# Optimization experiments

Measured on AMD Instinct MI355X. Metric: run time of the kernel, lower is better.

The kernel has to match this reference:

```python
import jax, jax.numpy as jnp
import numpy as np

L, N, E, D = 4, 50000, 250000, 128
EPS = 1e-5

def _ln(h, g, b):
    mu = jnp.mean(h, axis=-1, keepdims=True)
    var = jnp.mean(jnp.square(h - mu), axis=-1, keepdims=True)
    return (h - mu) * jax.lax.rsqrt(var + EPS) * g + b

def setup_inputs() -> dict:
    key = jax.random.key(0)
    ks = jax.random.split(key, 8)
    s1 = 1.0 / np.sqrt(3 * D)
    s2 = 1.0 / np.sqrt(D)
    s3 = 1.0 / np.sqrt(2 * D)
    return {
        "x": jax.random.normal(ks[0], (N, D), jnp.float32),
        "edge_index": jax.random.randint(ks[1], (2, E), 0, N, jnp.int32),
        "edge_attr": jax.random.normal(ks[2], (E, D), jnp.float32),
        "eW1": jax.random.normal(ks[3], (L, 3 * D, D), jnp.float32) * s1,
        "eb1": jnp.zeros((L, D), jnp.float32),
        "eW2": jax.random.normal(ks[4], (L, D, D), jnp.float32) * s2,
        "eb2": jnp.zeros((L, D), jnp.float32),
        "eG": jnp.ones((L, D), jnp.float32),
        "eB": jnp.zeros((L, D), jnp.float32),
        "nW1": jax.random.normal(ks[5], (L, 2 * D, D), jnp.float32) * s3,
        "nb1": jnp.zeros((L, D), jnp.float32),
        "nW2": jax.random.normal(ks[6], (L, D, D), jnp.float32) * s2,
        "nb2": jnp.zeros((L, D), jnp.float32),
        "nG": jnp.ones((L, D), jnp.float32),
        "nB": jnp.zeros((L, D), jnp.float32),
    }

def reference(x, edge_index, edge_attr, eW1, eb1, eW2, eb2, eG, eB,
              nW1, nb1, nW2, nb2, nG, nB):
    src = edge_index[0]  # scatter target (custom aggregate uses edge_index[0])
    dst = edge_index[1]  # x_i under PyG source_to_target flow
    n_nodes = x.shape[0]

    def step(carry, p):
        xc, ea = carry
        ew1, eb1_, ew2, eb2_, eg, ebt, nw1, nb1_, nw2, nb2_, ng, nbt = p
        # message: cat(x_i, x_j, edge_attr) -> MLP -> residual
        m = jnp.concatenate([xc[dst], xc[src], ea], axis=1)  # [E, 3D]
        h = jax.nn.relu(m @ ew1 + eb1_) @ ew2 + eb2_
        ea_new = ea + _ln(h, eg, ebt)
        # aggregate: scatter-sum edges into nodes by edge_index[0]
        agg = jax.ops.segment_sum(ea_new, src, num_segments=n_nodes)  # [N, D]
        # update: cat(x, agg) -> MLP -> residual
        u = jnp.concatenate([xc, agg], axis=1)  # [N, 2D]
        h2 = jax.nn.relu(u @ nw1 + nb1_) @ nw2 + nb2_
        x_new = xc + _ln(h2, ng, nbt)
        return (x_new, ea_new), None

    (x_out, ea_out), _ = jax.lax.scan(
        step, (x, edge_attr),
        (eW1, eb1, eW2, eb2, eG, eB, nW1, nb1, nW2, nb2, nG, nB))
    return x_out, ea_out
```

## Files before the change

kernel.cpp:

```cpp
#include <hip/hip_runtime.h>
#include <hip/hip_bf16.h>

#define N_NODES 50000
#define N_EDGES 250000
#define DIM 128
#define LAYERS 4
#define LN_EPS 1e-5f

typedef __hip_bfloat16 bf16;
typedef float f32x4 __attribute__((ext_vector_type(4)));
typedef __bf16 bfx8 __attribute__((ext_vector_type(8)));
typedef unsigned short u16x8 __attribute__((ext_vector_type(8)));
typedef unsigned short u16x4 __attribute__((ext_vector_type(4)));
typedef unsigned int   u32x4 __attribute__((ext_vector_type(4)));

#define F_X   0
#define F_EA  1
#define F_EW1 2
#define F_EW2 3
#define F_EG  4
#define F_NW1 5
#define F_NW2 6
#define F_NG  7

__device__ __forceinline__ float b2f(bf16 v) { return __bfloat162float(v); }
__device__ __forceinline__ bf16  f2b(float v) { return __float2bfloat16(v); }
__device__ __forceinline__ unsigned short f2us(float v) {
    return __builtin_bit_cast(unsigned short, __float2bfloat16(v));
}
__device__ __forceinline__ float us2f(unsigned short u) {
    return __builtin_bit_cast(float, (unsigned)u << 16);
}

__device__ __forceinline__ float ldv(const void* p, size_t i, int f) {
    if (f) return ((const float*)p)[i];
    else   return b2f(((const bf16*)p)[i]);
}
__device__ __forceinline__ void stv(void* p, size_t i, float v, int f) {
    if (f) ((float*)p)[i] = v;
    else   ((bf16*)p)[i] = f2b(v);
}

__device__ __forceinline__ bfx8 cvt8(f32x4 lo, f32x4 hi) {
    u16x8 u;
    #pragma unroll
    for (int i = 0; i < 4; i++) { u[i] = f2us(lo[i]); u[i + 4] = f2us(hi[i]); }
    return __builtin_bit_cast(bfx8, u);
}

__device__ __forceinline__ void mfma8(const bf16* pBk, bfx8 a, f32x4* acc) {
    #pragma unroll
    for (int f = 0; f < 8; f++) {
        bfx8 b = *reinterpret_cast<const bfx8*>(pBk + f * 128);
        acc[f] = __builtin_amdgcn_mfma_f32_16x16x32_bf16(a, b, acc[f], 0, 0, 0);
    }
}

__global__ void k_detect(const void* x, const void* ea,
                         const void* eW1, const void* eW2,
                         const void* nW1, const void* nW2,
                         const void* eG, const void* nG,
                         int* flags)
{
    __shared__ int bad[6];
    const void* ptrs[6] = { x, ea, eW1, eW2, nW1, nW2 };
    const int t = threadIdx.x;
    if (t < 6) bad[t] = 0;
    __syncthreads();
    for (int b = 0; b < 6; b++) {
        const bf16* p = (const bf16*)ptrs[b];
        int isbad = 0;
        for (int i = t; i < 4096; i += 256) {
            float v = b2f(p[i]);
            if (!(fabsf(v) < 1e4f)) isbad = 1;
        }
        if (isbad) atomicOr(&bad[b], 1);
    }
    __syncthreads();
    if (t == 0) {
        flags[F_X]   = bad[0];
        flags[F_EA]  = bad[1];
        flags[F_EW1] = bad[2];
        flags[F_EW2] = bad[3];
        flags[F_NW1] = bad[4];
        flags[F_NW2] = bad[5];
        const bf16* g1 = (const bf16*)eG;
        const bf16* g2 = (const bf16*)nG;
        flags[F_EG] = (b2f(g1[0]) == 1.0f && b2f(g1[1]) == 1.0f) ? 0 : 1;
        flags[F_NG] = (b2f(g2[0]) == 1.0f && b2f(g2[1]) == 1.0f) ? 0 : 1;
    }
}

__global__ void k_init_x(const void* __restrict__ x_in, float* __restrict__ xf,
                         bf16* __restrict__ xb, const int* __restrict__ flags) {
    const int f = flags[F_X];
    size_t i = ((size_t)blockIdx.x * 256 + threadIdx.x) * 4;
    if (i >= (size_t)N_NODES * DIM) return;
    f32x4 v;
    if (f) {
        v = *(const f32x4*)((const float*)x_in + i);
    } else {
        u16x4 u = *(const u16x4*)((const unsigned short*)x_in + i);
        #pragma unroll
        for (int q = 0; q < 4; q++) v[q] = us2f(u[q]);
    }
    *(f32x4*)(xf + i) = v;
    u16x4 ub;
    #pragma unroll
    for (int q = 0; q < 4; q++) ub[q] = f2us(v[q]);
    *(u16x4*)((unsigned short*)xb + i) = ub;
}

__global__ void k_init_ea(const void* __restrict__ ea_in, void* __restrict__ d_out,
                          const int* __restrict__ flags) {
    const int fe = flags[F_EA];
    const int fo = flags[F_X];
    size_t i = ((size_t)blockIdx.x * 256 + threadIdx.x) * 4;
    if (i >= (size_t)N_EDGES * DIM) return;
    if (fe == fo) {
        if (fo) {
            float* d = (float*)d_out + (size_t)N_NODES * DIM;
            *(u32x4*)(d + i) = *(const u32x4*)((const float*)ea_in + i);
        } else {
            bf16* d = (bf16*)d_out + (size_t)N_NODES * DIM;
            *(u16x4*)((unsigned short*)d + i) =
                *(const u16x4*)((const unsigned short*)ea_in + i);
        }
    } else {
        f32x4 v;
        if (fe) v = *(const f32x4*)((const float*)ea_in + i);
        else {
            u16x4 u = *(const u16x4*)((const unsigned short*)ea_in + i);
            #pragma unroll
            for (int q = 0; q < 4; q++) v[q] = us2f(u[q]);
        }
        if (fo) {
            float* d = (float*)d_out + (size_t)N_NODES * DIM;
            *(f32x4*)(d + i) = v;
        } else {
            bf16* d = (bf16*)d_out + (size_t)N_NODES * DIM;
            u16x4 ub;
            #pragma unroll
            for (int q = 0; q < 4; q++) ub[q] = f2us(v[q]);
            *(u16x4*)((unsigned short*)d + i) = ub;
        }
    }
}

__global__ void k_wprep(const void* __restrict__ W, bf16* __restrict__ Wb,
                        int K, const int* __restrict__ flags, int fidx)
{
    const int f = flags[fidx];
    size_t i = (size_t)blockIdx.x * 256 + threadIdx.x;
    const int per = K * DIM;
    if (i >= (size_t)LAYERS * per) return;
    int l   = (int)(i / per);
    int rem = (int)(i % per);
    int j   = rem & 7;
    int c   = (rem >> 3) & 127;
    int kq  = rem >> 10;
    int k   = kq * 8 + j;
    Wb[i] = f2b(ldv(W, (size_t)l * per + (size_t)k * DIM + c, f));
}

__global__ void k_deg(const int* __restrict__ srcI, int* __restrict__ deg) {
    int e = blockIdx.x * 256 + threadIdx.x;
    if (e < N_EDGES) atomicAdd(&deg[srcI[e]], 1);
}

#define SCH ((N_NODES + 255) / 256)
__global__ void k_scan(const int* __restrict__ deg, int* __restrict__ off,
                       int* __restrict__ cur) {
    __shared__ int part[256];
    const int t = threadIdx.x;
    const int lo = t * SCH;
    const int hi = (lo + SCH < N_NODES) ? (lo + SCH) : N_NODES;
    int s = 0;
    for (int i = lo; i < hi; i++) s += deg[i];
    part[t] = s;
    __syncthreads();
    if (t == 0) {
        int run = 0;
        for (int i = 0; i < 256; i++) { int v = part[i]; part[i] = run; run += v; }
    }
    __syncthreads();
    int run = part[t];
    for (int i = lo; i < hi; i++) { off[i] = run; cur[i] = run; run += deg[i]; }
    if (hi == N_NODES) off[N_NODES] = run;
}

__global__ void k_fill(const int* __restrict__ srcI, int* __restrict__ cur,
                       int* __restrict__ lst) {
    int e = blockIdx.x * 256 + threadIdx.x;
    if (e < N_EDGES) {
        int p = atomicAdd(&cur[srcI[e]], 1);
        lst[p] = e;
    }
}

__global__ __launch_bounds__(256)
void k_edge(const bf16* __restrict__ xb,
            void* __restrict__ d_out,
            const int* __restrict__ srcI, const int* __restrict__ dstI,
            const bf16* __restrict__ W1b, const bf16* __restrict__ W2b,
            const void* __restrict__ b1, const void* __restrict__ b2,
            const void* __restrict__ G,  const void* __restrict__ B,
            const int* __restrict__ flags, int layer)
{
    __shared__ alignas(16) float smem[4][16 * 132];

    const int fo = flags[F_X];
    const int fg = flags[F_EG];

    void* ea = fo ? (void*)((float*)d_out + (size_t)N_NODES * DIM)
                  : (void*)((bf16*)d_out + (size_t)N_NODES * DIM);

    const bf16* W1l = W1b + (size_t)layer * 3 * DIM * DIM;
    const bf16* W2l = W2b + (size_t)layer * DIM * DIM;
    const bf16* b1l = (const bf16*)b1 + (size_t)layer * DIM;
    const bf16* b2l = (const bf16*)b2 + (size_t)layer * DIM;
    const bf16* Bl  = (const bf16*)B  + (size_t)layer * DIM;
    const void* Gl  = fg ? (const void*)((const float*)G + (size_t)layer * DIM)
                         : (const void*)((const bf16*)G  + (size_t)layer * DIM);

    const int tid  = threadIdx.x;
    const int wv   = tid >> 6;
    const int lane = tid & 63;
    const int cl   = lane & 15;
    const int kp   = lane >> 4;

    const int e0w = blockIdx.x * 64 + wv * 16;
    const int eA  = (e0w + cl < N_EDGES) ? (e0w + cl) : (N_EDGES - 1);
    const bf16* pAd = xb + (size_t)dstI[eA] * DIM + kp * 8;
    const bf16* pAs = xb + (size_t)srcI[eA] * DIM + kp * 8;
    const bf16* pB  = W1l + kp * 1024 + cl * 8;

    f32x4 acc[8];
    #pragma unroll
    for (int f = 0; f < 8; f++) acc[f] = (f32x4){0.f, 0.f, 0.f, 0.f};

    #pragma unroll
    for (int kk = 0; kk < 4; kk++)
        mfma8(pB + (size_t)kk * 4096,
              *reinterpret_cast<const bfx8*>(pAd + kk * 32), acc);
    #pragma unroll
    for (int kk = 0; kk < 4; kk++)
        mfma8(pB + (size_t)(kk + 4) * 4096,
              *reinterpret_cast<const bfx8*>(pAs + kk * 32), acc);
    if (fo) {
        const float* pAe = (const float*)ea + (size_t)eA * DIM + kp * 8;
        #pragma unroll
        for (int kk = 0; kk < 4; kk++) {
            f32x4 lo = *reinterpret_cast<const f32x4*>(pAe + kk * 32);
            f32x4 hi = *reinterpret_cast<const f32x4*>(pAe + kk * 32 + 4);
            mfma8(pB + (size_t)(kk + 8) * 4096, cvt8(lo, hi), acc);
        }
    } else {
        const bf16* pAe = (const bf16*)ea + (size_t)eA * DIM + kp * 8;
        #pragma unroll
        for (int kk = 0; kk < 4; kk++)
            mfma8(pB + (size_t)(kk + 8) * 4096,
                  *reinterpret_cast<const bfx8*>(pAe + kk * 32), acc);
    }

    char* hb = (char*)&smem[wv][0];
    #pragma unroll
    for (int f = 0; f < 8; f++) {
        const int col = f * 16 + cl;
        const float bias1 = b2f(b1l[col]);
        #pragma unroll
        for (int j = 0; j < 4; j++) {
            const int r = kp * 4 + j;
            float hv = fmaxf(acc[f][j] + bias1, 0.f);
            *(bf16*)(hb + r * 256 + ((col * 2) ^ ((r & 7) << 4))) = f2b(hv);
        }
    }

    const bf16* pB2 = W2l + kp * 1024 + cl * 8;
    f32x4 acc2[8];
    #pragma unroll
    for (int f = 0; f < 8; f++) acc2[f] = (f32x4){0.f, 0.f, 0.f, 0.f};
    #pragma unroll
    for (int kk = 0; kk < 4; kk++) {
        bfx8 a = *reinterpret_cast<const bfx8*>(
            hb + cl * 256 + ((kk * 64 + kp * 16) ^ ((cl & 7) << 4)));
        mfma8(pB2 + (size_t)kk * 4096, a, acc2);
    }

    float g_[8], be_[8];
    #pragma unroll
    for (int f = 0; f < 8; f++) {
        const int col = f * 16 + cl;
        const float bias2 = b2f(b2l[col]);
        #pragma unroll
        for (int j = 0; j < 4; j++) acc2[f][j] += bias2;
        g_[f]  = ldv(Gl, col, fg);
        be_[f] = b2f(Bl[col]);
    }
    float mu[4], rs[4];
    #pragma unroll
    for (int j = 0; j < 4; j++) {
        float s = 0.f, q = 0.f;
        #pragma unroll
        for (int f = 0; f < 8; f++) { float v = acc2[f][j]; s += v; q += v * v; }
        #pragma unroll
        for (int m = 1; m <= 8; m <<= 1) { s += __shfl_xor(s, m); q += __shfl_xor(q, m); }
        mu[j] = s * (1.f / DIM);
        float var = q * (1.f / DIM) - mu[j] * mu[j];
        rs[j] = rsqrtf(var + LN_EPS);
    }

    float* vs = &smem[wv][0];
    #pragma unroll
    for (int f = 0; f < 8; f++) {
        #pragma unroll
        for (int j = 0; j < 4; j++) {
            const float val = (acc2[f][j] - mu[j]) * rs[j] * g_[f] + be_[f];
            vs[(kp * 4 + j) * 132 + f * 16 + cl] = val;
        }
    }
    const int lr = lane >> 5;
    const int lc = (lane & 31) * 4;
    #pragma unroll
    for (int i = 0; i < 8; i++) {
        const int r2 = 2 * i + lr;
        const int e  = e0w + r2;
        if (e >= N_EDGES) continue;
        f32x4 v = *(const f32x4*)&vs[r2 * 132 + lc];
        const size_t off = (size_t)e * DIM + lc;
        if (fo) {
            float* pe = (float*)ea + off;
            f32x4 o = *(const f32x4*)pe;
            *(f32x4*)pe = o + v;
        } else {
            bf16* pe = (bf16*)ea + off;
            u16x4 uo = *(const u16x4*)(unsigned short*)pe;
            u16x4 un;
            #pragma unroll
            for (int q = 0; q < 4; q++) un[q] = f2us(us2f(uo[q]) + v[q]);
            *(u16x4*)(unsigned short*)pe = un;
        }
    }
}

__global__ __launch_bounds__(256)
void k_node(float* __restrict__ xf, bf16* __restrict__ xb,
            void* __restrict__ d_out,
            const int* __restrict__ off_, const int* __restrict__ lst,
            const bf16* __restrict__ W1b, const bf16* __restrict__ W2b,
            const void* __restrict__ b1, const void* __restrict__ b2,
            const void* __restrict__ G,  const void* __restrict__ B,
            const int* __restrict__ flags, int layer)
{
    __shared__ alignas(16) float smem[4][16 * 132];

    const int fo = flags[F_X];
    const int fg = flags[F_NG];

    const bf16* W1l = W1b + (size_t)layer * 2 * DIM * DIM;
    const bf16* W2l = W2b + (size_t)layer * DIM * DIM;
    const bf16* b1l = (const bf16*)b1 + (size_t)layer * DIM;
    const bf16* b2l = (const bf16*)b2 + (size_t)layer * DIM;
    const bf16* Bl  = (const bf16*)B  + (size_t)layer * DIM;
    const void* Gl  = fg ? (const void*)((const float*)G + (size_t)layer * DIM)
                         : (const void*)((const bf16*)G  + (size_t)layer * DIM);

    const int tid  = threadIdx.x;
    const int wv   = tid >> 6;
    const int lane = tid & 63;
    const int cl   = lane & 15;
    const int kp   = lane >> 4;

    const int n0w = blockIdx.x * 64 + wv * 16;
    const int nA  = (n0w + cl < N_NODES) ? (n0w + cl) : (N_NODES - 1);

    f32x4 agl[4], agh[4];
    #pragma unroll
    for (int kk = 0; kk < 4; kk++) {
        agl[kk] = (f32x4){0.f, 0.f, 0.f, 0.f};
        agh[kk] = (f32x4){0.f, 0.f, 0.f, 0.f};
    }
    {
        const int beg = off_[nA], end = off_[nA + 1];
        if (fo) {
            const float* base = (const float*)d_out + (size_t)N_NODES * DIM;
            for (int idx = beg; idx < end; ++idx) {
                const int e = lst[idx];
                const float* p = base + (size_t)e * DIM + kp * 8;
                #pragma unroll
                for (int kk = 0; kk < 4; kk++) {
                    agl[kk] += *(const f32x4*)(p + kk * 32);
                    agh[kk] += *(const f32x4*)(p + kk * 32 + 4);
                }
            }
        } else {
            const bf16* base = (const bf16*)d_out + (size_t)N_NODES * DIM;
            for (int idx = beg; idx < end; ++idx) {
                const int e = lst[idx];
                const bf16* p = base + (size_t)e * DIM + kp * 8;
                #pragma unroll
                for (int kk = 0; kk < 4; kk++) {
                    u16x8 u = *(const u16x8*)(const unsigned short*)(p + kk * 32);
                    #pragma unroll
                    for (int q = 0; q < 4; q++) {
                        agl[kk][q] += us2f(u[q]);
                        agh[kk][q] += us2f(u[q + 4]);
                    }
                }
            }
        }
    }

    const bf16* pAx = xb + (size_t)nA * DIM + kp * 8;
    const bf16* pB  = W1l + kp * 1024 + cl * 8;

    f32x4 acc[8];
    #pragma unroll
    for (int f = 0; f < 8; f++) acc[f] = (f32x4){0.f, 0.f, 0.f, 0.f};

    #pragma unroll
    for (int kk = 0; kk < 4; kk++)
        mfma8(pB + (size_t)kk * 4096,
              *reinterpret_cast<const bfx8*>(pAx + kk * 32), acc);
    #pragma unroll
    for (int kk = 0; kk < 4; kk++)
        mfma8(pB + (size_t)(kk + 4) * 4096, cvt8(agl[kk], agh[kk]), acc);

    char* hb = (char*)&smem[wv][0];
    #pragma unroll
    for (int f = 0; f < 8; f++) {
        const int col = f * 16 + cl;
        const float bias1 = b2f(b1l[col]);
        #pragma unroll
        for (int j = 0; j < 4; j++) {
            const int r = kp * 4 + j;
            float hv = fmaxf(acc[f][j] + bias1, 0.f);
            *(bf16*)(hb + r * 256 + ((col * 2) ^ ((r & 7) << 4))) = f2b(hv);
        }
    }

    const bf16* pB2 = W2l + kp * 1024 + cl * 8;
    f32x4 acc2[8];
    #pragma unroll
    for (int f = 0; f < 8; f++) acc2[f] = (f32x4){0.f, 0.f, 0.f, 0.f};
    #pragma unroll
    for (int kk = 0; kk < 4; kk++) {
        bfx8 a = *reinterpret_cast<const bfx8*>(
            hb + cl * 256 + ((kk * 64 + kp * 16) ^ ((cl & 7) << 4)));
        mfma8(pB2 + (size_t)kk * 4096, a, acc2);
    }

    float g_[8], be_[8];
    #pragma unroll
    for (int f = 0; f < 8; f++) {
        const int col = f * 16 + cl;
        const float bias2 = b2f(b2l[col]);
        #pragma unroll
        for (int j = 0; j < 4; j++) acc2[f][j] += bias2;
        g_[f]  = ldv(Gl, col, fg);
        be_[f] = b2f(Bl[col]);
    }
    float mu[4], rs[4];
    #pragma unroll
    for (int j = 0; j < 4; j++) {
        float s = 0.f, q = 0.f;
        #pragma unroll
        for (int f = 0; f < 8; f++) { float v = acc2[f][j]; s += v; q += v * v; }
        #pragma unroll
        for (int m = 1; m <= 8; m <<= 1) { s += __shfl_xor(s, m); q += __shfl_xor(q, m); }
        mu[j] = s * (1.f / DIM);
        float var = q * (1.f / DIM) - mu[j] * mu[j];
        rs[j] = rsqrtf(var + LN_EPS);
    }

    float* vs = &smem[wv][0];
    #pragma unroll
    for (int f = 0; f < 8; f++) {
        #pragma unroll
        for (int j = 0; j < 4; j++) {
            const float val = (acc2[f][j] - mu[j]) * rs[j] * g_[f] + be_[f];
            vs[(kp * 4 + j) * 132 + f * 16 + cl] = val;
        }
    }
    const bool wout = (layer == LAYERS - 1);
    const int lr = lane >> 5;
    const int lc = (lane & 31) * 4;
    #pragma unroll
    for (int i = 0; i < 8; i++) {
        const int r2 = 2 * i + lr;
        const int n2 = n0w + r2;
        if (n2 >= N_NODES) continue;
        f32x4 v = *(const f32x4*)&vs[r2 * 132 + lc];
        const size_t off = (size_t)n2 * DIM + lc;
        f32x4 xo = *(const f32x4*)&xf[off];
        f32x4 xn = xo + v;
        *(f32x4*)&xf[off] = xn;
        u16x4 ub;
        #pragma unroll
        for (int q = 0; q < 4; q++) ub[q] = f2us(xn[q]);
        *(u16x4*)((unsigned short*)xb + off) = ub;
        if (wout) {
            if (fo) *(f32x4*)((float*)d_out + off) = xn;
            else    *(u16x4*)((unsigned short*)(bf16*)d_out + off) = ub;
        }
    }
}

extern "C" void kernel_launch(void* const* d_in, const int* in_sizes, int n_in,
                              void* d_out, int out_size, void* d_ws, size_t ws_size,
                              hipStream_t stream)
{
    (void)in_sizes; (void)n_in; (void)out_size; (void)ws_size;
    const void* x_in  = d_in[0];
    const int*  ei    = (const int*)d_in[1];
    const void* ea_in = d_in[2];
    const void* eW1 = d_in[3];  const void* eb1 = d_in[4];
    const void* eW2 = d_in[5];  const void* eb2 = d_in[6];
    const void* eG  = d_in[7];  const void* eB  = d_in[8];
    const void* nW1 = d_in[9];  const void* nb1 = d_in[10];
    const void* nW2 = d_in[11]; const void* nb2 = d_in[12];
    const void* nG  = d_in[13]; const void* nB  = d_in[14];

    char* ws = (char*)d_ws;
    int* flags = (int*)ws;
    char* p = ws + 256;
    float* xf  = (float*)p;  p += (size_t)N_NODES * DIM * 4;
    bf16*  xb  = (bf16*)p;   p += (size_t)N_NODES * DIM * 2;
    bf16*  eW1b = (bf16*)p;  p += (size_t)LAYERS * 3 * DIM * DIM * 2;
    bf16*  eW2b = (bf16*)p;  p += (size_t)LAYERS * DIM * DIM * 2;
    bf16*  nW1b = (bf16*)p;  p += (size_t)LAYERS * 2 * DIM * DIM * 2;
    bf16*  nW2b = (bf16*)p;  p += (size_t)LAYERS * DIM * DIM * 2;
    int* deg     = (int*)p;  p += 200000;
    int* csr_off = (int*)p;  p += 200016;
    int* cur     = (int*)p;  p += 200000;
    int* lst     = (int*)p;  p += 1000000;

    const int* srcI = ei;
    const int* dstI = ei + N_EDGES;

    k_detect<<<1, 256, 0, stream>>>(x_in, ea_in, eW1, eW2, nW1, nW2, eG, nG, flags);
    k_init_x<<<(N_NODES * DIM / 4 + 255) / 256, 256, 0, stream>>>(x_in, xf, xb, flags);
    k_init_ea<<<(int)(((size_t)N_EDGES * DIM / 4 + 255) / 256), 256, 0, stream>>>(ea_in, d_out, flags);
    k_wprep<<<(LAYERS * 3 * DIM * DIM + 255) / 256, 256, 0, stream>>>(eW1, eW1b, 3 * DIM, flags, F_EW1);
    k_wprep<<<(LAYERS * DIM * DIM + 255) / 256, 256, 0, stream>>>(eW2, eW2b, DIM, flags, F_EW2);
    k_wprep<<<(LAYERS * 2 * DIM * DIM + 255) / 256, 256, 0, stream>>>(nW1, nW1b, 2 * DIM, flags, F_NW1);
    k_wprep<<<(LAYERS * DIM * DIM + 255) / 256, 256, 0, stream>>>(nW2, nW2b, DIM, flags, F_NW2);

    hipMemsetAsync(deg, 0, N_NODES * sizeof(int), stream);
    k_deg<<<(N_EDGES + 255) / 256, 256, 0, stream>>>(srcI, deg);
    k_scan<<<1, 256, 0, stream>>>(deg, csr_off, cur);
    k_fill<<<(N_EDGES + 255) / 256, 256, 0, stream>>>(srcI, cur, lst);

    for (int l = 0; l < LAYERS; l++) {
        k_edge<<<(N_EDGES + 63) / 64, 256, 0, stream>>>(
            xb, d_out, srcI, dstI, eW1b, eW2b, eb1, eb2, eG, eB, flags, l);
        k_node<<<(N_NODES + 63) / 64, 256, 0, stream>>>(
            xf, xb, d_out, csr_off, lst, nW1b, nW2b, nb1, nb2, nG, nB, flags, l);
    }
}
```

Before: 1.392 ms.

## Write edge outputs in CSR-sorted bf16 copy for contiguous node aggregation

The edge kernel now also writes each updated edge feature, rounded to bf16, into an extra buffer at its CSR position. The node kernel can then stream each node's incoming edges contiguously instead of gathering through an index list. The old edge-attribute values are also prefetched at the start of the edge kernel so their latency overlaps the matmuls. In exchange the edge kernel does an extra scattered bf16 write, uses more workspace, and in fp32 mode the node aggregation now sums bf16-rounded values, which costs precision.

After: 2.069 ms. +48.6%, slower.

```diff
diff --git a/kernel.cpp b/kernel.cpp
--- a/kernel.cpp
+++ b/kernel.cpp
@@ -190,11 +190,11 @@
 }
 
 __global__ void k_fill(const int* __restrict__ srcI, int* __restrict__ cur,
-                       int* __restrict__ lst) {
+                       int* __restrict__ pos) {
     int e = blockIdx.x * 256 + threadIdx.x;
     if (e < N_EDGES) {
         int p = atomicAdd(&cur[srcI[e]], 1);
-        lst[p] = e;
+        pos[e] = p;
     }
 }
 
@@ -202,6 +202,7 @@
 void k_edge(const bf16* __restrict__ xb,
             void* __restrict__ d_out,
             const int* __restrict__ srcI, const int* __restrict__ dstI,
+            const int* __restrict__ pos,  bf16* __restrict__ eac,
             const bf16* __restrict__ W1b, const bf16* __restrict__ W2b,
             const void* __restrict__ b1, const void* __restrict__ b2,
             const void* __restrict__ G,  const void* __restrict__ B,
@@ -214,6 +215,28 @@
 
     void* ea = fo ? (void*)((float*)d_out + (size_t)N_NODES * DIM)
                   : (void*)((bf16*)d_out + (size_t)N_NODES * DIM);
+
+    const int tid  = threadIdx.x;
+    const int wv   = tid >> 6;
+    const int lane = tid & 63;
+    const int cl   = lane & 15;
+    const int kp   = lane >> 4;
+
+    const int e0w = blockIdx.x * 64 + wv * 16;
+
+    const int lr = lane >> 5;
+    const int lc = (lane & 31) * 4;
+    f32x4 eaof[8];
+    u16x4 eaob[8];
+    int   posR[8];
+    #pragma unroll
+    for (int i = 0; i < 8; i++) {
+        const int e = e0w + 2 * i + lr;
+        const int ec = (e < N_EDGES) ? e : (N_EDGES - 1);
+        posR[i] = pos[ec];
+        if (fo) eaof[i] = *(const f32x4*)((const float*)ea + (size_t)ec * DIM + lc);
+        else    eaob[i] = *(const u16x4*)((const unsigned short*)ea + (size_t)ec * DIM + lc);
+    }
 
     const bf16* W1l = W1b + (size_t)layer * 3 * DIM * DIM;
     const bf16* W2l = W2b + (size_t)layer * DIM * DIM;
@@ -223,13 +246,6 @@
     const void* Gl  = fg ? (const void*)((const float*)G + (size_t)layer * DIM)
                          : (const void*)((const bf16*)G  + (size_t)layer * DIM);
 
-    const int tid  = threadIdx.x;
-    const int wv   = tid >> 6;
-    const int lane = tid & 63;
-    const int cl   = lane & 15;
-    const int kp   = lane >> 4;
-
-    const int e0w = blockIdx.x * 64 + wv * 16;
     const int eA  = (e0w + cl < N_EDGES) ? (e0w + cl) : (N_EDGES - 1);
     const bf16* pAd = xb + (size_t)dstI[eA] * DIM + kp * 8;
     const bf16* pAs = xb + (size_t)srcI[eA] * DIM + kp * 8;
@@ -319,8 +335,6 @@
             vs[(kp * 4 + j) * 132 + f * 16 + cl] = val;
         }
     }
-    const int lr = lane >> 5;
-    const int lc = (lane & 31) * 4;
     #pragma unroll
     for (int i = 0; i < 8; i++) {
         const int r2 = 2 * i + lr;
@@ -328,25 +342,26 @@
         if (e >= N_EDGES) continue;
         f32x4 v = *(const f32x4*)&vs[r2 * 132 + lc];
         const size_t off = (size_t)e * DIM + lc;
+        f32x4 nw;
         if (fo) {
-            float* pe = (float*)ea + off;
-            f32x4 o = *(const f32x4*)pe;
-            *(f32x4*)pe = o + v;
+            nw = eaof[i] + v;
+            *(f32x4*)((float*)ea + off) = nw;
         } else {
-            bf16* pe = (bf16*)ea + off;
-            u16x4 uo = *(const u16x4*)(unsigned short*)pe;
-            u16x4 un;
             #pragma unroll
-            for (int q = 0; q < 4; q++) un[q] = f2us(us2f(uo[q]) + v[q]);
-            *(u16x4*)(unsigned short*)pe = un;
-        }
+            for (int q = 0; q < 4; q++) nw[q] = us2f(eaob[i][q]) + v[q];
+        }
+        u16x4 ub;
+        #pragma unroll
+        for (int q = 0; q < 4; q++) ub[q] = f2us(nw[q]);
+        if (!fo) *(u16x4*)((unsigned short*)ea + off) = ub;
+        *(u16x4*)((unsigned short*)eac + (size_t)posR[i] * DIM + lc) = ub;
     }
 }
 
 __global__ __launch_bounds__(256)
 void k_node(float* __restrict__ xf, bf16* __restrict__ xb,
             void* __restrict__ d_out,
-            const int* __restrict__ off_, const int* __restrict__ lst,
+            const int* __restrict__ off_, const bf16* __restrict__ eac,
             const bf16* __restrict__ W1b, const bf16* __restrict__ W2b,
             const void* __restrict__ b1, const void* __restrict__ b2,
             const void* __restrict__ G,  const void* __restrict__ B,
@@ -382,30 +397,16 @@
     }
     {
         const int beg = off_[nA], end = off_[nA + 1];
-        if (fo) {
-            const float* base = (const float*)d_out + (size_t)N_NODES * DIM;
-            for (int idx = beg; idx < end; ++idx) {
-                const int e = lst[idx];
-                const float* p = base + (size_t)e * DIM + kp * 8;
+        const unsigned short* pr =
+            (const unsigned short*)eac + (size_t)beg * DIM + kp * 8;
+        for (int idx = beg; idx < end; ++idx, pr += DIM) {
+            #pragma unroll
+            for (int kk = 0; kk < 4; kk++) {
+                u16x8 u = *(const u16x8*)(pr + kk * 32);
                 #pragma unroll
-                for (int kk = 0; kk < 4; kk++) {
-                    agl[kk] += *(const f32x4*)(p + kk * 32);
-                    agh[kk] += *(const f32x4*)(p + kk * 32 + 4);
-                }
-            }
-        } else {
-            const bf16* base = (const bf16*)d_out + (size_t)N_NODES * DIM;
-            for (int idx = beg; idx < end; ++idx) {
-                const int e = lst[idx];
-                const bf16* p = base + (size_t)e * DIM + kp * 8;
-                #pragma unroll
-                for (int kk = 0; kk < 4; kk++) {
-                    u16x8 u = *(const u16x8*)(const unsigned short*)(p + kk * 32);
-                    #pragma unroll
-                    for (int q = 0; q < 4; q++) {
-                        agl[kk][q] += us2f(u[q]);
-                        agh[kk][q] += us2f(u[q + 4]);
-                    }
+                for (int q = 0; q < 4; q++) {
+                    agl[kk][q] += us2f(u[q]);
+                    agh[kk][q] += us2f(u[q + 4]);
                 }
             }
         }
@@ -533,7 +534,8 @@
     int* deg     = (int*)p;  p += 200000;
     int* csr_off = (int*)p;  p += 200016;
     int* cur     = (int*)p;  p += 200000;
-    int* lst     = (int*)p;  p += 1000000;
+    int* pos     = (int*)p;  p += 1000000;
+    bf16* eac    = (bf16*)p; p += (size_t)N_EDGES * DIM * 2;
 
     const int* srcI = ei;
     const int* dstI = ei + N_EDGES;
@@ -549,12 +551,12 @@
     hipMemsetAsync(deg, 0, N_NODES * sizeof(int), stream);
     k_deg<<<(N_EDGES + 255) / 256, 256, 0, stream>>>(srcI, deg);
     k_scan<<<1, 256, 0, stream>>>(deg, csr_off, cur);
-    k_fill<<<(N_EDGES + 255) / 256, 256, 0, stream>>>(srcI, cur, lst);
+    k_fill<<<(N_EDGES + 255) / 256, 256, 0, stream>>>(srcI, cur, pos);
 
     for (int l = 0; l < LAYERS; l++) {
         k_edge<<<(N_EDGES + 63) / 64, 256, 0, stream>>>(
-            xb, d_out, srcI, dstI, eW1b, eW2b, eb1, eb2, eG, eB, flags, l);
+            xb, d_out, srcI, dstI, pos, eac, eW1b, eW2b, eb1, eb2, eG, eB, flags, l);
         k_node<<<(N_NODES + 63) / 64, 256, 0, stream>>>(
-            xf, xb, d_out, csr_off, lst, nW1b, nW2b, nb1, nb2, nG, nB, flags, l);
-    }
-}
+            xf, xb, d_out, csr_off, eac, nW1b, nW2b, nb1, nb2, nG, nB, flags, l);
+    }
+}
```

## Store edge features in CSR-sorted order so node aggregation reads contiguously

Applied to the files above, without the earlier changes.

Edge attributes are permuted into a float32 workspace sorted by scatter target (CSR order), with src/dst indices permuted to match. The node kernel now sums a contiguous run of rows instead of gathering rows through the edge list, and the edge kernel writes results back in sorted order. The final layer scatters results back to the original edge order in the output. This adds a permutation pass, extra workspace, and a scattered write on the last layer, and it keeps edge state in fp32 even when the output is bf16.

Result: slower. 1.972 ms (+41.6%).

```diff
diff --git a/kernel.cpp b/kernel.cpp
--- a/kernel.cpp
+++ b/kernel.cpp
@@ -35,10 +35,6 @@
 __device__ __forceinline__ float ldv(const void* p, size_t i, int f) {
     if (f) return ((const float*)p)[i];
     else   return b2f(((const bf16*)p)[i]);
-}
-__device__ __forceinline__ void stv(void* p, size_t i, float v, int f) {
-    if (f) ((float*)p)[i] = v;
-    else   ((bf16*)p)[i] = f2b(v);
 }
 
 __device__ __forceinline__ bfx8 cvt8(f32x4 lo, f32x4 hi) {
@@ -111,40 +107,24 @@
     *(u16x4*)((unsigned short*)xb + i) = ub;
 }
 
-__global__ void k_init_ea(const void* __restrict__ ea_in, void* __restrict__ d_out,
+__global__ void k_init_ea(const void* __restrict__ ea_in, float* __restrict__ eaw,
+                          const int* __restrict__ lst,
                           const int* __restrict__ flags) {
     const int fe = flags[F_EA];
-    const int fo = flags[F_X];
     size_t i = ((size_t)blockIdx.x * 256 + threadIdx.x) * 4;
     if (i >= (size_t)N_EDGES * DIM) return;
-    if (fe == fo) {
-        if (fo) {
-            float* d = (float*)d_out + (size_t)N_NODES * DIM;
-            *(u32x4*)(d + i) = *(const u32x4*)((const float*)ea_in + i);
-        } else {
-            bf16* d = (bf16*)d_out + (size_t)N_NODES * DIM;
-            *(u16x4*)((unsigned short*)d + i) =
-                *(const u16x4*)((const unsigned short*)ea_in + i);
-        }
-    } else {
-        f32x4 v;
-        if (fe) v = *(const f32x4*)((const float*)ea_in + i);
-        else {
-            u16x4 u = *(const u16x4*)((const unsigned short*)ea_in + i);
-            #pragma unroll
-            for (int q = 0; q < 4; q++) v[q] = us2f(u[q]);
-        }
-        if (fo) {
-            float* d = (float*)d_out + (size_t)N_NODES * DIM;
-            *(f32x4*)(d + i) = v;
-        } else {
-            bf16* d = (bf16*)d_out + (size_t)N_NODES * DIM;
-            u16x4 ub;
-            #pragma unroll
-            for (int q = 0; q < 4; q++) ub[q] = f2us(v[q]);
-            *(u16x4*)((unsigned short*)d + i) = ub;
-        }
-    }
+    const int p   = (int)(i >> 7);
+    const int col = (int)(i & 127);
+    const int e   = lst[p];
+    const size_t si = (size_t)e * DIM + col;
+    f32x4 v;
+    if (fe) v = *(const f32x4*)((const float*)ea_in + si);
+    else {
+        u16x4 u = *(const u16x4*)((const unsigned short*)ea_in + si);
+        #pragma unroll
+        for (int q = 0; q < 4; q++) v[q] = us2f(u[q]);
+    }
+    *(f32x4*)(eaw + i) = v;
 }
 
 __global__ void k_wprep(const void* __restrict__ W, bf16* __restrict__ Wb,
@@ -198,10 +178,23 @@
     }
 }
 
+__global__ void k_perm(const int* __restrict__ srcI, const int* __restrict__ dstI,
+                       const int* __restrict__ lst,
+                       int* __restrict__ srcP, int* __restrict__ dstP) {
+    int p = blockIdx.x * 256 + threadIdx.x;
+    if (p < N_EDGES) {
+        const int e = lst[p];
+        srcP[p] = srcI[e];
+        dstP[p] = dstI[e];
+    }
+}
+
 __global__ __launch_bounds__(256)
 void k_edge(const bf16* __restrict__ xb,
+            float* __restrict__ eaw,
             void* __restrict__ d_out,
-            const int* __restrict__ srcI, const int* __restrict__ dstI,
+            const int* __restrict__ srcP, const int* __restrict__ dstP,
+            const int* __restrict__ lst,
             const bf16* __restrict__ W1b, const bf16* __restrict__ W2b,
             const void* __restrict__ b1, const void* __restrict__ b2,
             const void* __restrict__ G,  const void* __restrict__ B,
@@ -211,9 +204,6 @@
 
     const int fo = flags[F_X];
     const int fg = flags[F_EG];
-
-    void* ea = fo ? (void*)((float*)d_out + (size_t)N_NODES * DIM)
-                  : (void*)((bf16*)d_out + (size_t)N_NODES * DIM);
 
     const bf16* W1l = W1b + (size_t)layer * 3 * DIM * DIM;
     const bf16* W2l = W2b + (size_t)layer * DIM * DIM;
@@ -230,9 +220,11 @@
     const int kp   = lane >> 4;
 
     const int e0w = blockIdx.x * 64 + wv * 16;
-    const int eA  = (e0w + cl < N_EDGES) ? (e0w + cl) : (N_EDGES - 1);
-    const bf16* pAd = xb + (size_t)dstI[eA] * DIM + kp * 8;
-    const bf16* pAs = xb + (size_t)srcI[eA] * DIM + kp * 8;
+
+    const int pA  = (e0w + cl < N_EDGES) ? (e0w + cl) : (N_EDGES - 1);
+    const bf16* pAd = xb + (size_t)dstP[pA] * DIM + kp * 8;
+    const bf16* pAs = xb + (size_t)srcP[pA] * DIM + kp * 8;
+    const float* pAe = eaw + (size_t)pA * DIM + kp * 8;
     const bf16* pB  = W1l + kp * 1024 + cl * 8;
 
     f32x4 acc[8];
@@ -247,20 +239,11 @@
     for (int kk = 0; kk < 4; kk++)
         mfma8(pB + (size_t)(kk + 4) * 4096,
               *reinterpret_cast<const bfx8*>(pAs + kk * 32), acc);
-    if (fo) {
-        const float* pAe = (const float*)ea + (size_t)eA * DIM + kp * 8;
-        #pragma unroll
-        for (int kk = 0; kk < 4; kk++) {
-            f32x4 lo = *reinterpret_cast<const f32x4*>(pAe + kk * 32);
-            f32x4 hi = *reinterpret_cast<const f32x4*>(pAe + kk * 32 + 4);
-            mfma8(pB + (size_t)(kk + 8) * 4096, cvt8(lo, hi), acc);
-        }
-    } else {
-        const bf16* pAe = (const bf16*)ea + (size_t)eA * DIM + kp * 8;
-        #pragma unroll
-        for (int kk = 0; kk < 4; kk++)
-            mfma8(pB + (size_t)(kk + 8) * 4096,
-                  *reinterpret_cast<const bfx8*>(pAe + kk * 32), acc);
+    #pragma unroll
+    for (int kk = 0; kk < 4; kk++) {
+        f32x4 lo = *reinterpret_cast<const f32x4*>(pAe + kk * 32);
+        f32x4 hi = *reinterpret_cast<const f32x4*>(pAe + kk * 32 + 4);
+        mfma8(pB + (size_t)(kk + 8) * 4096, cvt8(lo, hi), acc);
     }
 
     char* hb = (char*)&smem[wv][0];
@@ -319,26 +302,31 @@
             vs[(kp * 4 + j) * 132 + f * 16 + cl] = val;
         }
     }
+    const bool last = (layer == LAYERS - 1);
     const int lr = lane >> 5;
     const int lc = (lane & 31) * 4;
     #pragma unroll
     for (int i = 0; i < 8; i++) {
         const int r2 = 2 * i + lr;
-        const int e  = e0w + r2;
-        if (e >= N_EDGES) continue;
+        const int p  = e0w + r2;
+        if (p >= N_EDGES) continue;
         f32x4 v = *(const f32x4*)&vs[r2 * 132 + lc];
-        const size_t off = (size_t)e * DIM + lc;
-        if (fo) {
-            float* pe = (float*)ea + off;
-            f32x4 o = *(const f32x4*)pe;
-            *(f32x4*)pe = o + v;
-        } else {
-            bf16* pe = (bf16*)ea + off;
-            u16x4 uo = *(const u16x4*)(unsigned short*)pe;
-            u16x4 un;
-            #pragma unroll
-            for (int q = 0; q < 4; q++) un[q] = f2us(us2f(uo[q]) + v[q]);
-            *(u16x4*)(unsigned short*)pe = un;
+        float* pe = eaw + (size_t)p * DIM + lc;
+        f32x4 o = *(const f32x4*)pe;
+        f32x4 nw = o + v;
+        *(f32x4*)pe = nw;
+        if (last) {
+            const size_t off = (size_t)lst[p] * DIM + lc;
+            if (fo) {
+                float* d = (float*)d_out + (size_t)N_NODES * DIM;
+                *(f32x4*)(d + off) = nw;
+            } else {
+                bf16* d = (bf16*)d_out + (size_t)N_NODES * DIM;
+                u16x4 ub;
+                #pragma unroll
+                for (int q = 0; q < 4; q++) ub[q] = f2us(nw[q]);
+                *(u16x4*)((unsigned short*)d + off) = ub;
+            }
         }
     }
 }
@@ -346,7 +334,7 @@
 __global__ __launch_bounds__(256)
 void k_node(float* __restrict__ xf, bf16* __restrict__ xb,
             void* __restrict__ d_out,
-            const int* __restrict__ off_, const int* __restrict__ lst,
+            const int* __restrict__ off_, const float* __restrict__ eaw,
             const bf16* __restrict__ W1b, const bf16* __restrict__ W2b,
             const void* __restrict__ b1, const void* __restrict__ b2,
             const void* __restrict__ G,  const void* __restrict__ B,
@@ -382,31 +370,12 @@
     }
     {
         const int beg = off_[nA], end = off_[nA + 1];
-        if (fo) {
-            const float* base = (const float*)d_out + (size_t)N_NODES * DIM;
-            for (int idx = beg; idx < end; ++idx) {
-                const int e = lst[idx];
-                const float* p = base + (size_t)e * DIM + kp * 8;
-                #pragma unroll
-                for (int kk = 0; kk < 4; kk++) {
-                    agl[kk] += *(const f32x4*)(p + kk * 32);
-                    agh[kk] += *(const f32x4*)(p + kk * 32 + 4);
-                }
-            }
-        } else {
-            const bf16* base = (const bf16*)d_out + (size_t)N_NODES * DIM;
-            for (int idx = beg; idx < end; ++idx) {
-                const int e = lst[idx];
-                const bf16* p = base + (size_t)e * DIM + kp * 8;
-                #pragma unroll
-                for (int kk = 0; kk < 4; kk++) {
-                    u16x8 u = *(const u16x8*)(const unsigned short*)(p + kk * 32);
-                    #pragma unroll
-                    for (int q = 0; q < 4; q++) {
-                        agl[kk][q] += us2f(u[q]);
-                        agh[kk][q] += us2f(u[q + 4]);
-                    }
-                }
+        const float* pr = eaw + (size_t)beg * DIM + kp * 8;
+        for (int idx = beg; idx < end; ++idx, pr += DIM) {
+            #pragma unroll
+            for (int kk = 0; kk < 4; kk++) {
+                agl[kk] += *(const f32x4*)(pr + kk * 32);
+                agh[kk] += *(const f32x4*)(pr + kk * 32 + 4);
             }
         }
     }
@@ -534,13 +503,16 @@
     int* csr_off = (int*)p;  p += 200016;
     int* cur     = (int*)p;  p += 200000;
     int* lst     = (int*)p;  p += 1000000;
+    int* srcP    = (int*)p;  p += 1000000;
+    int* dstP    = (int*)p;  p += 1000000;
+    p = (char*)(((size_t)p + 255) & ~(size_t)255);
+    float* eaw   = (float*)p; p += (size_t)N_EDGES * DIM * 4;
 
     const int* srcI = ei;
     const int* dstI = ei + N_EDGES;
 
     k_detect<<<1, 256, 0, stream>>>(x_in, ea_in, eW1, eW2, nW1, nW2, eG, nG, flags);
     k_init_x<<<(N_NODES * DIM / 4 + 255) / 256, 256, 0, stream>>>(x_in, xf, xb, flags);
-    k_init_ea<<<(int)(((size_t)N_EDGES * DIM / 4 + 255) / 256), 256, 0, stream>>>(ea_in, d_out, flags);
     k_wprep<<<(LAYERS * 3 * DIM * DIM + 255) / 256, 256, 0, stream>>>(eW1, eW1b, 3 * DIM, flags, F_EW1);
     k_wprep<<<(LAYERS * DIM * DIM + 255) / 256, 256, 0, stream>>>(eW2, eW2b, DIM, flags, F_EW2);
     k_wprep<<<(LAYERS * 2 * DIM * DIM + 255) / 256, 256, 0, stream>>>(nW1, nW1b, 2 * DIM, flags, F_NW1);
@@ -550,11 +522,13 @@
     k_deg<<<(N_EDGES + 255) / 256, 256, 0, stream>>>(srcI, deg);
     k_scan<<<1, 256, 0, stream>>>(deg, csr_off, cur);
     k_fill<<<(N_EDGES + 255) / 256, 256, 0, stream>>>(srcI, cur, lst);
+    k_perm<<<(N_EDGES + 255) / 256, 256, 0, stream>>>(srcI, dstI, lst, srcP, dstP);
+    k_init_ea<<<(int)(((size_t)N_EDGES * DIM / 4 + 255) / 256), 256, 0, stream>>>(ea_in, eaw, lst, flags);
 
     for (int l = 0; l < LAYERS; l++) {
         k_edge<<<(N_EDGES + 63) / 64, 256, 0, stream>>>(
-            xb, d_out, srcI, dstI, eW1b, eW2b, eb1, eb2, eG, eB, flags, l);
+            xb, eaw, d_out, srcP, dstP, lst, eW1b, eW2b, eb1, eb2, eG, eB, flags, l);
         k_node<<<(N_NODES + 63) / 64, 256, 0, stream>>>(
-            xf, xb, d_out, csr_off, lst, nW1b, nW2b, nb1, nb2, nG, nB, flags, l);
-    }
-}
+            xf, xb, d_out, csr_off, eaw, nW1b, nW2b, nb1, nb2, nG, nB, flags, l);
+    }
+}
```

## Process two edge tiles per wave and stage node aggregation through LDS

Applied to the files above, without the earlier changes.

The edge kernel now handles 32 edges per wave, issuing two MFMA chains for each weight fragment. Each loaded W1/W2 fragment is reused twice, which halves weight traffic per edge at the cost of more accumulator registers and possibly lower occupancy. The node kernel now loads the block's contiguous CSR range of edge rows into shared memory in chunks of 64, with coalesced row loads and block-wide barriers. Each wave then sums its nodes' rows from LDS instead of doing per-lane scattered global gathers. The ea init kernel's same-type copy branch is also folded into the general convert path.

Measured after the change: 1.971 ms. 1.42x slower.

```diff
diff --git a/kernel.cpp b/kernel.cpp
--- a/kernel.cpp
+++ b/kernel.cpp
@@ -53,6 +53,16 @@
     for (int f = 0; f < 8; f++) {
         bfx8 b = *reinterpret_cast<const bfx8*>(pBk + f * 128);
         acc[f] = __builtin_amdgcn_mfma_f32_16x16x32_bf16(a, b, acc[f], 0, 0, 0);
+    }
+}
+
+__device__ __forceinline__ void mfma8d(const bf16* pBk, bfx8 a0, bfx8 a1,
+                                       f32x4* acc0, f32x4* acc1) {
+    #pragma unroll
+    for (int f = 0; f < 8; f++) {
+        bfx8 b = *reinterpret_cast<const bfx8*>(pBk + f * 128);
+        acc0[f] = __builtin_amdgcn_mfma_f32_16x16x32_bf16(a0, b, acc0[f], 0, 0, 0);
+        acc1[f] = __builtin_amdgcn_mfma_f32_16x16x32_bf16(a1, b, acc1[f], 0, 0, 0);
     }
 }
 
@@ -117,33 +127,22 @@
     const int fo = flags[F_X];
     size_t i = ((size_t)blockIdx.x * 256 + threadIdx.x) * 4;
     if (i >= (size_t)N_EDGES * DIM) return;
-    if (fe == fo) {
-        if (fo) {
-            float* d = (float*)d_out + (size_t)N_NODES * DIM;
-            *(u32x4*)(d + i) = *(const u32x4*)((const float*)ea_in + i);
-        } else {
-            bf16* d = (bf16*)d_out + (size_t)N_NODES * DIM;
-            *(u16x4*)((unsigned short*)d + i) =
-                *(const u16x4*)((const unsigned short*)ea_in + i);
-        }
+    f32x4 v;
+    if (fe) v = *(const f32x4*)((const float*)ea_in + i);
+    else {
+        u16x4 u = *(const u16x4*)((const unsigned short*)ea_in + i);
+        #pragma unroll
+        for (int q = 0; q < 4; q++) v[q] = us2f(u[q]);
+    }
+    if (fo) {
+        float* d = (float*)d_out + (size_t)N_NODES * DIM;
+        *(f32x4*)(d + i) = v;
     } else {
-        f32x4 v;
-        if (fe) v = *(const f32x4*)((const float*)ea_in + i);
-        else {
-            u16x4 u = *(const u16x4*)((const unsigned short*)ea_in + i);
-            #pragma unroll
-            for (int q = 0; q < 4; q++) v[q] = us2f(u[q]);
-        }
-        if (fo) {
-            float* d = (float*)d_out + (size_t)N_NODES * DIM;
-            *(f32x4*)(d + i) = v;
-        } else {
-            bf16* d = (bf16*)d_out + (size_t)N_NODES * DIM;
-            u16x4 ub;
-            #pragma unroll
-            for (int q = 0; q < 4; q++) ub[q] = f2us(v[q]);
-            *(u16x4*)((unsigned short*)d + i) = ub;
-        }
+        bf16* d = (bf16*)d_out + (size_t)N_NODES * DIM;
+        u16x4 ub;
+        #pragma unroll
+        for (int q = 0; q < 4; q++) ub[q] = f2us(v[q]);
+        *(u16x4*)((unsigned short*)d + i) = ub;
     }
 }
 
@@ -198,124 +197,28 @@
     }
 }
 
-__global__ __launch_bounds__(256)
-void k_edge(const bf16* __restrict__ xb,
-            void* __restrict__ d_out,
-            const int* __restrict__ srcI, const int* __restrict__ dstI,
-            const bf16* __restrict__ W1b, const bf16* __restrict__ W2b,
-            const void* __restrict__ b1, const void* __restrict__ b2,
-            const void* __restrict__ G,  const void* __restrict__ B,
-            const int* __restrict__ flags, int layer)
+__device__ __forceinline__ void edge_epi(
+    f32x4 (&c2)[8], const float* g_, const float* be_,
+    float* vs, void* ea, int fo, int e_base,
+    int lane, int cl, int kp)
 {
-    __shared__ alignas(16) float smem[4][16 * 132];
-
-    const int fo = flags[F_X];
-    const int fg = flags[F_EG];
-
-    void* ea = fo ? (void*)((float*)d_out + (size_t)N_NODES * DIM)
-                  : (void*)((bf16*)d_out + (size_t)N_NODES * DIM);
-
-    const bf16* W1l = W1b + (size_t)layer * 3 * DIM * DIM;
-    const bf16* W2l = W2b + (size_t)layer * DIM * DIM;
-    const bf16* b1l = (const bf16*)b1 + (size_t)layer * DIM;
-    const bf16* b2l = (const bf16*)b2 + (size_t)layer * DIM;
-    const bf16* Bl  = (const bf16*)B  + (size_t)layer * DIM;
-    const void* Gl  = fg ? (const void*)((const float*)G + (size_t)layer * DIM)
-                         : (const void*)((const bf16*)G  + (size_t)layer * DIM);
-
-    const int tid  = threadIdx.x;
-    const int wv   = tid >> 6;
-    const int lane = tid & 63;
-    const int cl   = lane & 15;
-    const int kp   = lane >> 4;
-
-    const int e0w = blockIdx.x * 64 + wv * 16;
-    const int eA  = (e0w + cl < N_EDGES) ? (e0w + cl) : (N_EDGES - 1);
-    const bf16* pAd = xb + (size_t)dstI[eA] * DIM + kp * 8;
-    const bf16* pAs = xb + (size_t)srcI[eA] * DIM + kp * 8;
-    const bf16* pB  = W1l + kp * 1024 + cl * 8;
-
-    f32x4 acc[8];
-    #pragma unroll
-    for (int f = 0; f < 8; f++) acc[f] = (f32x4){0.f, 0.f, 0.f, 0.f};
-
-    #pragma unroll
-    for (int kk = 0; kk < 4; kk++)
-        mfma8(pB + (size_t)kk * 4096,
-              *reinterpret_cast<const bfx8*>(pAd + kk * 32), acc);
-    #pragma unroll
-    for (int kk = 0; kk < 4; kk++)
-        mfma8(pB + (size_t)(kk + 4) * 4096,
-              *reinterpret_cast<const bfx8*>(pAs + kk * 32), acc);
-    if (fo) {
-        const float* pAe = (const float*)ea + (size_t)eA * DIM + kp * 8;
-        #pragma unroll
-        for (int kk = 0; kk < 4; kk++) {
-            f32x4 lo = *reinterpret_cast<const f32x4*>(pAe + kk * 32);
-            f32x4 hi = *reinterpret_cast<const f32x4*>(pAe + kk * 32 + 4);
-            mfma8(pB + (size_t)(kk + 8) * 4096, cvt8(lo, hi), acc);
-        }
-    } else {
-        const bf16* pAe = (const bf16*)ea + (size_t)eA * DIM + kp * 8;
-        #pragma unroll
-        for (int kk = 0; kk < 4; kk++)
-            mfma8(pB + (size_t)(kk + 8) * 4096,
-                  *reinterpret_cast<const bfx8*>(pAe + kk * 32), acc);
-    }
-
-    char* hb = (char*)&smem[wv][0];
-    #pragma unroll
-    for (int f = 0; f < 8; f++) {
-        const int col = f * 16 + cl;
-        const float bias1 = b2f(b1l[col]);
-        #pragma unroll
-        for (int j = 0; j < 4; j++) {
-            const int r = kp * 4 + j;
-            float hv = fmaxf(acc[f][j] + bias1, 0.f);
-            *(bf16*)(hb + r * 256 + ((col * 2) ^ ((r & 7) << 4))) = f2b(hv);
-        }
-    }
-
-    const bf16* pB2 = W2l + kp * 1024 + cl * 8;
-    f32x4 acc2[8];
-    #pragma unroll
-    for (int f = 0; f < 8; f++) acc2[f] = (f32x4){0.f, 0.f, 0.f, 0.f};
-    #pragma unroll
-    for (int kk = 0; kk < 4; kk++) {
-        bfx8 a = *reinterpret_cast<const bfx8*>(
-            hb + cl * 256 + ((kk * 64 + kp * 16) ^ ((cl & 7) << 4)));
-        mfma8(pB2 + (size_t)kk * 4096, a, acc2);
-    }
-
-    float g_[8], be_[8];
-    #pragma unroll
-    for (int f = 0; f < 8; f++) {
-        const int col = f * 16 + cl;
-        const float bias2 = b2f(b2l[col]);
-        #pragma unroll
-        for (int j = 0; j < 4; j++) acc2[f][j] += bias2;
-        g_[f]  = ldv(Gl, col, fg);
-        be_[f] = b2f(Bl[col]);
-    }
     float mu[4], rs[4];
     #pragma unroll
     for (int j = 0; j < 4; j++) {
         float s = 0.f, q = 0.f;
         #pragma unroll
-        for (int f = 0; f < 8; f++) { float v = acc2[f][j]; s += v; q += v * v; }
+        for (int f = 0; f < 8; f++) { float v = c2[f][j]; s += v; q += v * v; }
         #pragma unroll
         for (int m = 1; m <= 8; m <<= 1) { s += __shfl_xor(s, m); q += __shfl_xor(q, m); }
         mu[j] = s * (1.f / DIM);
         float var = q * (1.f / DIM) - mu[j] * mu[j];
         rs[j] = rsqrtf(var + LN_EPS);
     }
-
-    float* vs = &smem[wv][0];
     #pragma unroll
     for (int f = 0; f < 8; f++) {
         #pragma unroll
         for (int j = 0; j < 4; j++) {
-            const float val = (acc2[f][j] - mu[j]) * rs[j] * g_[f] + be_[f];
+            const float val = (c2[f][j] - mu[j]) * rs[j] * g_[f] + be_[f];
             vs[(kp * 4 + j) * 132 + f * 16 + cl] = val;
         }
     }
@@ -324,7 +227,7 @@
     #pragma unroll
     for (int i = 0; i < 8; i++) {
         const int r2 = 2 * i + lr;
-        const int e  = e0w + r2;
+        const int e  = e_base + r2;
         if (e >= N_EDGES) continue;
         f32x4 v = *(const f32x4*)&vs[r2 * 132 + lc];
         const size_t off = (size_t)e * DIM + lc;
@@ -344,6 +247,133 @@
 }
 
 __global__ __launch_bounds__(256)
+void k_edge(const bf16* __restrict__ xb,
+            void* __restrict__ d_out,
+            const int* __restrict__ srcI, const int* __restrict__ dstI,
+            const bf16* __restrict__ W1b, const bf16* __restrict__ W2b,
+            const void* __restrict__ b1, const void* __restrict__ b2,
+            const void* __restrict__ G,  const void* __restrict__ B,
+            const int* __restrict__ flags, int layer)
+{
+    __shared__ alignas(16) float smem[4][2112];
+
+    const int fo = flags[F_X];
+    const int fg = flags[F_EG];
+
+    void* ea = fo ? (void*)((float*)d_out + (size_t)N_NODES * DIM)
+                  : (void*)((bf16*)d_out + (size_t)N_NODES * DIM);
+
+    const bf16* W1l = W1b + (size_t)layer * 3 * DIM * DIM;
+    const bf16* W2l = W2b + (size_t)layer * DIM * DIM;
+    const bf16* b1l = (const bf16*)b1 + (size_t)layer * DIM;
+    const bf16* b2l = (const bf16*)b2 + (size_t)layer * DIM;
+    const bf16* Bl  = (const bf16*)B  + (size_t)layer * DIM;
+    const void* Gl  = fg ? (const void*)((const float*)G + (size_t)layer * DIM)
+                         : (const void*)((const bf16*)G  + (size_t)layer * DIM);
+
+    const int tid  = threadIdx.x;
+    const int wv   = tid >> 6;
+    const int lane = tid & 63;
+    const int cl   = lane & 15;
+    const int kp   = lane >> 4;
+
+    const int e0w = blockIdx.x * 128 + wv * 32;
+    const int eA0 = (e0w + cl      < N_EDGES) ? (e0w + cl)      : (N_EDGES - 1);
+    const int eA1 = (e0w + 16 + cl < N_EDGES) ? (e0w + 16 + cl) : (N_EDGES - 1);
+
+    const bf16* pAd0 = xb + (size_t)dstI[eA0] * DIM + kp * 8;
+    const bf16* pAs0 = xb + (size_t)srcI[eA0] * DIM + kp * 8;
+    const bf16* pAd1 = xb + (size_t)dstI[eA1] * DIM + kp * 8;
+    const bf16* pAs1 = xb + (size_t)srcI[eA1] * DIM + kp * 8;
+    const bf16* pB   = W1l + kp * 1024 + cl * 8;
+
+    f32x4 acc0[8], acc1[8];
+    #pragma unroll
+    for (int f = 0; f < 8; f++) {
+        acc0[f] = (f32x4){0.f, 0.f, 0.f, 0.f};
+        acc1[f] = (f32x4){0.f, 0.f, 0.f, 0.f};
+    }
+
+    #pragma unroll
+    for (int kk = 0; kk < 4; kk++)
+        mfma8d(pB + (size_t)kk * 4096,
+               *reinterpret_cast<const bfx8*>(pAd0 + kk * 32),
+               *reinterpret_cast<const bfx8*>(pAd1 + kk * 32), acc0, acc1);
+    #pragma unroll
+    for (int kk = 0; kk < 4; kk++)
+        mfma8d(pB + (size_t)(kk + 4) * 4096,
+               *reinterpret_cast<const bfx8*>(pAs0 + kk * 32),
+               *reinterpret_cast<const bfx8*>(pAs1 + kk * 32), acc0, acc1);
+    if (fo) {
+        const float* pAe0 = (const float*)ea + (size_t)eA0 * DIM + kp * 8;
+        const float* pAe1 = (const float*)ea + (size_t)eA1 * DIM + kp * 8;
+        #pragma unroll
+        for (int kk = 0; kk < 4; kk++) {
+            f32x4 l0 = *reinterpret_cast<const f32x4*>(pAe0 + kk * 32);
+            f32x4 h0 = *reinterpret_cast<const f32x4*>(pAe0 + kk * 32 + 4);
+            f32x4 l1 = *reinterpret_cast<const f32x4*>(pAe1 + kk * 32);
+            f32x4 h1 = *reinterpret_cast<const f32x4*>(pAe1 + kk * 32 + 4);
+            mfma8d(pB + (size_t)(kk + 8) * 4096, cvt8(l0, h0), cvt8(l1, h1),
+                   acc0, acc1);
+        }
+    } else {
+        const bf16* pAe0 = (const bf16*)ea + (size_t)eA0 * DIM + kp * 8;
+        const bf16* pAe1 = (const bf16*)ea + (size_t)eA1 * DIM + kp * 8;
+        #pragma unroll
+        for (int kk = 0; kk < 4; kk++)
+            mfma8d(pB + (size_t)(kk + 8) * 4096,
+                   *reinterpret_cast<const bfx8*>(pAe0 + kk * 32),
+                   *reinterpret_cast<const bfx8*>(pAe1 + kk * 32), acc0, acc1);
+    }
+
+    char* hb0 = (char*)&smem[wv][0];
+    char* hb1 = hb0 + 4224;
+    #pragma unroll
+    for (int f = 0; f < 8; f++) {
+        const int col = f * 16 + cl;
+        const float bias1 = b2f(b1l[col]);
+        #pragma unroll
+        for (int j = 0; j < 4; j++) {
+            const int r = kp * 4 + j;
+            float h0 = fmaxf(acc0[f][j] + bias1, 0.f);
+            float h1 = fmaxf(acc1[f][j] + bias1, 0.f);
+            const int boff = r * 256 + ((col * 2) ^ ((r & 7) << 4));
+            *(bf16*)(hb0 + boff) = f2b(h0);
+            *(bf16*)(hb1 + boff) = f2b(h1);
+        }
+    }
+
+    const bf16* pB2 = W2l + kp * 1024 + cl * 8;
+    f32x4 c20[8], c21[8];
+    #pragma unroll
+    for (int f = 0; f < 8; f++) {
+        c20[f] = (f32x4){0.f, 0.f, 0.f, 0.f};
+        c21[f] = (f32x4){0.f, 0.f, 0.f, 0.f};
+    }
+    #pragma unroll
+    for (int kk = 0; kk < 4; kk++) {
+        const int aoff = (kk * 64 + kp * 16) ^ ((cl & 7) << 4);
+        bfx8 a0 = *reinterpret_cast<const bfx8*>(hb0 + cl * 256 + aoff);
+        bfx8 a1 = *reinterpret_cast<const bfx8*>(hb1 + cl * 256 + aoff);
+        mfma8d(pB2 + (size_t)kk * 4096, a0, a1, c20, c21);
+    }
+
+    float g_[8], be_[8];
+    #pragma unroll
+    for (int f = 0; f < 8; f++) {
+        const int col = f * 16 + cl;
+        const float bias2 = b2f(b2l[col]);
+        #pragma unroll
+        for (int j = 0; j < 4; j++) { c20[f][j] += bias2; c21[f][j] += bias2; }
+        g_[f]  = ldv(Gl, col, fg);
+        be_[f] = b2f(Bl[col]);
+    }
+    float* vs = &smem[wv][0];
+    edge_epi(c20, g_, be_, vs, ea, fo, e0w,      lane, cl, kp);
+    edge_epi(c21, g_, be_, vs, ea, fo, e0w + 16, lane, cl, kp);
+}
+
+__global__ __launch_bounds__(256)
 void k_node(float* __restrict__ xf, bf16* __restrict__ xb,
             void* __restrict__ d_out,
             const int* __restrict__ off_, const int* __restrict__ lst,
@@ -352,7 +382,7 @@
             const void* __restrict__ G,  const void* __restrict__ B,
             const int* __restrict__ flags, int layer)
 {
-    __shared__ alignas(16) float smem[4][16 * 132];
+    __shared__ alignas(16) float smem[4][2112];
 
     const int fo = flags[F_X];
     const int fg = flags[F_NG];
@@ -374,42 +404,59 @@
     const int n0w = blockIdx.x * 64 + wv * 16;
     const int nA  = (n0w + cl < N_NODES) ? (n0w + cl) : (N_NODES - 1);
 
+    const int nb0 = blockIdx.x * 64;
+    const int nbH = (nb0 + 64 < N_NODES) ? (nb0 + 64) : N_NODES;
+    const int beg_blk = off_[nb0];
+    const int end_blk = off_[nbH];
+    const int begN = off_[nA], endN = off_[nA + 1];
+
     f32x4 agl[4], agh[4];
     #pragma unroll
     for (int kk = 0; kk < 4; kk++) {
         agl[kk] = (f32x4){0.f, 0.f, 0.f, 0.f};
         agh[kk] = (f32x4){0.f, 0.f, 0.f, 0.f};
     }
-    {
-        const int beg = off_[nA], end = off_[nA + 1];
-        if (fo) {
-            const float* base = (const float*)d_out + (size_t)N_NODES * DIM;
-            for (int idx = beg; idx < end; ++idx) {
-                const int e = lst[idx];
-                const float* p = base + (size_t)e * DIM + kp * 8;
+
+    float* stage = &smem[0][0];
+    const int srow = tid >> 2;
+    const int scol = (tid & 3) * 32;
+
+    for (int c0 = beg_blk; c0 < end_blk; c0 += 64) {
+        const int cnt = (end_blk - c0 < 64) ? (end_blk - c0) : 64;
+        __syncthreads();
+        if (srow < cnt) {
+            const int e = lst[c0 + srow];
+            float* dp = stage + srow * 132 + scol;
+            if (fo) {
+                const float* sp = (const float*)d_out + (size_t)N_NODES * DIM
+                                + (size_t)e * DIM + scol;
                 #pragma unroll
-                for (int kk = 0; kk < 4; kk++) {
-                    agl[kk] += *(const f32x4*)(p + kk * 32);
-                    agh[kk] += *(const f32x4*)(p + kk * 32 + 4);
+                for (int q = 0; q < 8; q++)
+                    *(f32x4*)(dp + q * 4) = *(const f32x4*)(sp + q * 4);
+            } else {
+                const unsigned short* sp = (const unsigned short*)d_out
+                                + (size_t)N_NODES * DIM + (size_t)e * DIM + scol;
+                #pragma unroll
+                for (int q = 0; q < 4; q++) {
+                    u16x8 u = *(const u16x8*)(sp + q * 8);
+                    #pragma unroll
+                    for (int r = 0; r < 8; r++) dp[q * 8 + r] = us2f(u[r]);
                 }
             }
-        } else {
-            const bf16* base = (const bf16*)d_out + (size_t)N_NODES * DIM;
-            for (int idx = beg; idx < end; ++idx) {
-                const int e = lst[idx];
-                const bf16* p = base + (size_t)e * DIM + kp * 8;
-                #pragma unroll
-                for (int kk = 0; kk < 4; kk++) {
-                    u16x8 u = *(const u16x8*)(const unsigned short*)(p + kk * 32);
-                    #pragma unroll
-                    for (int q = 0; q < 4; q++) {
-                        agl[kk][q] += us2f(u[q]);
-                        agh[kk][q] += us2f(u[q + 4]);
-                    }
-                }
+        }
+        __syncthreads();
+        const int lo = (begN > c0) ? begN : c0;
+        const int hi = (endN < c0 + cnt) ? endN : (c0 + cnt);
+        for (int idx = lo - c0; idx < hi - c0; ++idx) {
+            const float* pr = stage + idx * 132 + kp * 8;
+            #pragma unroll
+            for (int kk = 0; kk < 4; kk++) {
+                agl[kk] += *(const f32x4*)(pr + kk * 32);
+                agh[kk] += *(const f32x4*)(pr + kk * 32 + 4);
             }
         }
     }
+    __syncthreads();
 
     const bf16* pAx = xb + (size_t)nA * DIM + kp * 8;
     const bf16* pB  = W1l + kp * 1024 + cl * 8;
@@ -552,7 +599,7 @@
     k_fill<<<(N_EDGES + 255) / 256, 256, 0, stream>>>(srcI, cur, lst);
 
     for (int l = 0; l < LAYERS; l++) {
-        k_edge<<<(N_EDGES + 63) / 64, 256, 0, stream>>>(
+        k_edge<<<(N_EDGES + 127) / 128, 256, 0, stream>>>(
             xb, d_out, srcI, dstI, eW1b, eW2b, eb1, eb2, eG, eB, flags, l);
         k_node<<<(N_NODES + 63) / 64, 256, 0, stream>>>(
             xf, xb, d_out, csr_off, lst, nW1b, nW2b, nb1, nb2, nG, nB, flags, l);
```
